# Kernel optimization log

Hardware: AMD Instinct MI355X
Metric: run time of the kernel (lower is better)

The kernel has to match this reference:

```python
import jax, jax.numpy as jnp
import numpy as np

NUM_CLASSES = 1000
ETA = 1e-6  # Constants.eta (small stabilizer)
N, D = 262144, 256


def setup_inputs() -> dict:
    key = jax.random.key(0)
    k1, k2 = jax.random.split(key)
    features = jax.random.normal(k1, (N, D), dtype=jnp.float32)
    labels = jax.random.randint(k2, (N,), 0, NUM_CLASSES, dtype=jnp.int32)
    conf_mat = jnp.zeros((NUM_CLASSES, NUM_CLASSES), dtype=jnp.float32)
    return {"features": features, "labels": labels, "conf_mat": conf_mat}


def reference(features, labels, conf_mat):
    C = NUM_CLASSES
    # --- per-class centroids via segment reduce (replaces per-class mask loop) ---
    counts = jax.ops.segment_sum(jnp.ones((features.shape[0],), features.dtype),
                                 labels, num_segments=C)            # [C]
    sums = jax.ops.segment_sum(features, labels, num_segments=C)    # [C, D]
    means = sums / jnp.maximum(counts, 1.0)[:, None]                # [C, D]

    # --- weighted between-class scatter list (sb_list from get_scatters) ---
    gmean = jnp.mean(features, axis=0)                              # [D]
    w = counts / features.shape[0]
    sb_list = w * jnp.sum((means - gmean) ** 2, axis=1)             # [C]

    # --- cosine distance between centroids ---
    mn = means / jnp.linalg.norm(means, axis=1, keepdims=True)      # L2-normalize rows
    dist = 1.0 - jnp.clip(mn @ mn.T, -1.0, 1.0)                     # [C, C]
    dist = dist.at[jnp.diag_indices(C)].set(jnp.inf)                # fill_diagonal_(inf)

    # first (row-major) position of the minimum == nonzero(dist == min)[0]
    flat = jnp.argmin(dist)
    i, j = flat // C, flat % C
    min_dist = jnp.where(i == j, jnp.sum(sb_list), dist[i, j])

    loss = jnp.log(1.0 / (min_dist + ETA) + 1.0)
    return loss
```

## Files before the change

### kernel.cpp

```cpp
#include <hip/hip_runtime.h>
#include <math.h>

#define N_ROWS 262144
#define D 256
#define C 1000
#define CAP 512
#define TILE 32
#define NTILE 32
#define NPAIR (NTILE * (NTILE + 1) / 2)

typedef float f4v __attribute__((ext_vector_type(4)));

__global__ void k_init(int* __restrict__ cnt, unsigned int* __restrict__ minb,
                       unsigned int* __restrict__ done) {
    int t = threadIdx.x;
    cnt[t] = 0;
    if (t == 0) *minb = 0x7f800000u;
    if (t == 1) *done = 0u;
}

__global__ void k_build(const int4* __restrict__ lab4, int* __restrict__ cnt,
                        int* __restrict__ list) {
    int i = blockIdx.x * 256 + threadIdx.x;
    int4 l = lab4[i];
    int base = i * 4;
    list[l.x * CAP + atomicAdd(&cnt[l.x], 1)] = base;
    list[l.y * CAP + atomicAdd(&cnt[l.y], 1)] = base + 1;
    list[l.z * CAP + atomicAdd(&cnt[l.z], 1)] = base + 2;
    list[l.w * CAP + atomicAdd(&cnt[l.w], 1)] = base + 3;
}

__global__ __launch_bounds__(512) void k_centroid(
    const float* __restrict__ feat, const int* __restrict__ list,
    const int* __restrict__ cnt, float* __restrict__ mn) {
    int c = blockIdx.x;
    int tid = threadIdx.x;
    int w = tid >> 6;
    int cg_ = tid & 63;
    int n = cnt[c];
    int nl = (n < CAP) ? n : CAP;

    __shared__ int srow[CAP];
    for (int i = tid; i < nl; i += 512) srow[i] = list[c * CAP + i];
    __syncthreads();

    f4v acc = {0.f, 0.f, 0.f, 0.f};
    int r = w;
    for (; r + 56 < nl; r += 64) {
        int rows[8];
        #pragma unroll
        for (int u = 0; u < 8; ++u) rows[u] = srow[r + u * 8];
        f4v v[8];
        #pragma unroll
        for (int u = 0; u < 8; ++u)
            v[u] = reinterpret_cast<const f4v*>(feat + (size_t)rows[u] * D)[cg_];
        #pragma unroll
        for (int u = 0; u < 8; ++u) acc += v[u];
    }
    for (; r < nl; r += 8) {
        int row = srow[r];
        acc += reinterpret_cast<const f4v*>(feat + (size_t)row * D)[cg_];
    }

    __shared__ f4v part[8][64];
    part[w][cg_] = acc;
    __syncthreads();
    if (w == 0) {
        f4v t = {0.f, 0.f, 0.f, 0.f};
        #pragma unroll
        for (int i = 0; i < 8; ++i) t += part[i][cg_];
        float inv = 1.0f / fmaxf((float)n, 1.0f);
        f4v mean = t * inv;
        float ss = mean.x * mean.x + mean.y * mean.y + mean.z * mean.z + mean.w * mean.w;
        #pragma unroll
        for (int o = 32; o; o >>= 1) ss += __shfl_down(ss, o, 64);
        ss = __shfl(ss, 0, 64);
        float rn = rsqrtf(ss);
        f4v o4 = mean * rn;
        reinterpret_cast<f4v*>(mn + (size_t)c * D)[cg_] = o4;
    }
}

__global__ __launch_bounds__(256) void k_mindist(
    const float* __restrict__ mn, unsigned int* __restrict__ minb,
    unsigned int* __restrict__ done, float* __restrict__ out) {
    int t = blockIdx.x;
    int bi = 0;
    while (t >= NTILE - bi) { t -= NTILE - bi; ++bi; }
    int bj = bi + t;
    int i0 = bi * TILE, j0 = bj * TILE;

    __shared__ float A[TILE * D];
    __shared__ float B[TILE * D];
    float4* A4 = reinterpret_cast<float4*>(A);
    float4* B4 = reinterpret_cast<float4*>(B);
    int tid = threadIdx.x;

    for (int k = tid; k < TILE * (D / 4); k += 256) {
        int r = k >> 6;
        int g = k & 63;
        int sg = g ^ ((r >> 1) & 7);
        int gi = i0 + r, gj = j0 + r;
        float4 z = make_float4(0.f, 0.f, 0.f, 0.f);
        A4[r * 64 + sg] = (gi < C) ? reinterpret_cast<const float4*>(mn + (size_t)gi * D)[g] : z;
        B4[r * 64 + sg] = (gj < C) ? reinterpret_cast<const float4*>(mn + (size_t)gj * D)[g] : z;
    }
    __syncthreads();

    int ti = tid >> 4, tj = tid & 15;
    int il = ti * 2, jl = tj * 2;
    int sa = ti & 7;
    int sb = tj & 7;

    float a00 = 0.f, a01 = 0.f, a10 = 0.f, a11 = 0.f;
    #pragma unroll 4
    for (int g = 0; g < 64; ++g) {
        float4 x0 = A4[il * 64 + (g ^ sa)];
        float4 x1 = A4[(il + 1) * 64 + (g ^ sa)];
        float4 y0 = B4[jl * 64 + (g ^ sb)];
        float4 y1 = B4[(jl + 1) * 64 + (g ^ sb)];
        a00 += x0.x * y0.x + x0.y * y0.y + x0.z * y0.z + x0.w * y0.w;
        a01 += x0.x * y1.x + x0.y * y1.y + x0.z * y1.z + x0.w * y1.w;
        a10 += x1.x * y0.x + x1.y * y0.y + x1.z * y0.z + x1.w * y0.w;
        a11 += x1.x * y1.x + x1.y * y1.y + x1.z * y1.z + x1.w * y1.w;
    }

    float m = INFINITY;
    int gi0 = i0 + il, gj0 = j0 + jl;
    if (gi0 < C && gj0 < C && gi0 != gj0)         m = fminf(m, 1.f - fminf(fmaxf(a00, -1.f), 1.f));
    if (gi0 < C && gj0 + 1 < C && gi0 != gj0 + 1) m = fminf(m, 1.f - fminf(fmaxf(a01, -1.f), 1.f));
    if (gi0 + 1 < C && gj0 < C && gi0 + 1 != gj0) m = fminf(m, 1.f - fminf(fmaxf(a10, -1.f), 1.f));
    if (gi0 + 1 < C && gj0 + 1 < C && gi0 != gj0) m = fminf(m, 1.f - fminf(fmaxf(a11, -1.f), 1.f));

    #pragma unroll
    for (int o = 32; o; o >>= 1) m = fminf(m, __shfl_down(m, o, 64));
    if ((tid & 63) == 0) atomicMin(minb, __float_as_uint(m));

    __syncthreads();
    if (tid == 0) {
        __threadfence();
        unsigned int old = atomicAdd(done, 1u);
        if (old == (unsigned int)(gridDim.x - 1)) {
            float d = __uint_as_float(atomicOr(minb, 0u));
            out[0] = logf(1.0f / (d + 1e-6f) + 1.0f);
        }
    }
}

extern "C" void kernel_launch(void* const* d_in, const int* in_sizes, int n_in,
                              void* d_out, int out_size, void* d_ws, size_t ws_size,
                              hipStream_t stream) {
    const float* feat   = (const float*)d_in[0];
    const int*   labels = (const int*)d_in[1];
    float* out = (float*)d_out;

    int*      cnt  = (int*)d_ws;
    int*      list = cnt + 1024;
    float*    mnrm = (float*)(list + C * CAP);
    unsigned* minb = (unsigned*)(mnrm + C * D);
    unsigned* done = minb + 1;

    k_init<<<1, 1024, 0, stream>>>(cnt, minb, done);
    k_build<<<N_ROWS / 4 / 256, 256, 0, stream>>>((const int4*)labels, cnt, list);
    k_centroid<<<C, 512, 0, stream>>>(feat, list, cnt, mnrm);
    k_mindist<<<NPAIR, 256, 0, stream>>>(mnrm, minb, done, out);
}
```

Measured before the change: 151.8 us.

## Replace list-based gather centroids with slab-partitioned shared-memory atomic segment sums

Drops the per-class row-list build and the gather kernel. Each block now streams a slab of rows and a 32-column group into a shared-memory accumulator of all classes, using LDS atomics, then writes the partial sums. A second kernel reduces the 32 slab partials per class and normalises the rows. Dividing by the count is skipped because it cancels under L2 normalisation. This removes the CAP truncation and the random row gathers, but adds about 33 MB of partial-sum traffic and heavy LDS atomic contention; init of minb/done is folded into block 0.

```diff
diff --git a/kernel.cpp b/kernel.cpp
--- a/kernel.cpp
+++ b/kernel.cpp
@@ -4,81 +4,78 @@
 #define N_ROWS 262144
 #define D 256
 #define C 1000
-#define CAP 512
+#define SLABS 32
+#define RPS (N_ROWS / SLABS)
+#define COLG 8
+#define PSTRIDE (C * 32)
 #define TILE 32
 #define NTILE 32
 #define NPAIR (NTILE * (NTILE + 1) / 2)
 
 typedef float f4v __attribute__((ext_vector_type(4)));
 
-__global__ void k_init(int* __restrict__ cnt, unsigned int* __restrict__ minb,
-                       unsigned int* __restrict__ done) {
-    int t = threadIdx.x;
-    cnt[t] = 0;
-    if (t == 0) *minb = 0x7f800000u;
-    if (t == 1) *done = 0u;
+__global__ __launch_bounds__(1024) void k_partial(
+    const float* __restrict__ feat, const int* __restrict__ labels,
+    float* __restrict__ partial, unsigned int* __restrict__ minb,
+    unsigned int* __restrict__ done) {
+    int b = blockIdx.x;
+    int s = b >> 3;
+    int g = b & 7;
+    int tid = threadIdx.x;
+    int row_off = tid >> 5;
+    int col = tid & 31;
+
+    if (b == 0) {
+        if (tid == 0) *minb = 0x7f800000u;
+        if (tid == 1) *done = 0u;
+    }
+
+    __shared__ float acc[C * 32];
+    for (int i = tid; i < C * 32; i += 1024) acc[i] = 0.f;
+    __syncthreads();
+
+    int base0 = s * RPS + row_off;
+    int colbase = g * 32 + col;
+    for (int it = 0; it < RPS / 256; ++it) {
+        int base = base0 + it * 256;
+        int cls[8];
+        float v[8];
+        #pragma unroll
+        for (int u = 0; u < 8; ++u) {
+            int r = base + u * 32;
+            cls[u] = labels[r];
+            v[u] = feat[(size_t)r * D + colbase];
+        }
+        #pragma unroll
+        for (int u = 0; u < 8; ++u)
+            atomicAdd(&acc[cls[u] * 32 + col], v[u]);
+    }
+    __syncthreads();
+
+    f4v* p4 = reinterpret_cast<f4v*>(partial + (size_t)b * PSTRIDE);
+    const f4v* a4 = reinterpret_cast<const f4v*>(acc);
+    for (int i = tid; i < PSTRIDE / 4; i += 1024) p4[i] = a4[i];
 }
 
-__global__ void k_build(const int4* __restrict__ lab4, int* __restrict__ cnt,
-                        int* __restrict__ list) {
-    int i = blockIdx.x * 256 + threadIdx.x;
-    int4 l = lab4[i];
-    int base = i * 4;
-    list[l.x * CAP + atomicAdd(&cnt[l.x], 1)] = base;
-    list[l.y * CAP + atomicAdd(&cnt[l.y], 1)] = base + 1;
-    list[l.z * CAP + atomicAdd(&cnt[l.z], 1)] = base + 2;
-    list[l.w * CAP + atomicAdd(&cnt[l.w], 1)] = base + 3;
-}
+__global__ __launch_bounds__(256) void k_norm(
+    const float* __restrict__ partial, float* __restrict__ mn) {
+    int c = blockIdx.x;
+    int d = threadIdx.x;
+    int g = d >> 5, cl = d & 31;
 
-__global__ __launch_bounds__(512) void k_centroid(
-    const float* __restrict__ feat, const int* __restrict__ list,
-    const int* __restrict__ cnt, float* __restrict__ mn) {
-    int c = blockIdx.x;
-    int tid = threadIdx.x;
-    int w = tid >> 6;
-    int cg_ = tid & 63;
-    int n = cnt[c];
-    int nl = (n < CAP) ? n : CAP;
+    float sum = 0.f;
+    #pragma unroll 4
+    for (int s = 0; s < SLABS; ++s)
+        sum += partial[(size_t)(s * COLG + g) * PSTRIDE + c * 32 + cl];
 
-    __shared__ int srow[CAP];
-    for (int i = tid; i < nl; i += 512) srow[i] = list[c * CAP + i];
+    float ss = sum * sum;
+    #pragma unroll
+    for (int o = 32; o; o >>= 1) ss += __shfl_down(ss, o, 64);
+    __shared__ float w[4];
+    if ((d & 63) == 0) w[d >> 6] = ss;
     __syncthreads();
-
-    f4v acc = {0.f, 0.f, 0.f, 0.f};
-    int r = w;
-    for (; r + 56 < nl; r += 64) {
-        int rows[8];
-        #pragma unroll
-        for (int u = 0; u < 8; ++u) rows[u] = srow[r + u * 8];
-        f4v v[8];
-        #pragma unroll
-        for (int u = 0; u < 8; ++u)
-            v[u] = reinterpret_cast<const f4v*>(feat + (size_t)rows[u] * D)[cg_];
-        #pragma unroll
-        for (int u = 0; u < 8; ++u) acc += v[u];
-    }
-    for (; r < nl; r += 8) {
-        int row = srow[r];
-        acc += reinterpret_cast<const f4v*>(feat + (size_t)row * D)[cg_];
-    }
-
-    __shared__ f4v part[8][64];
-    part[w][cg_] = acc;
-    __syncthreads();
-    if (w == 0) {
-        f4v t = {0.f, 0.f, 0.f, 0.f};
-        #pragma unroll
-        for (int i = 0; i < 8; ++i) t += part[i][cg_];
-        float inv = 1.0f / fmaxf((float)n, 1.0f);
-        f4v mean = t * inv;
-        float ss = mean.x * mean.x + mean.y * mean.y + mean.z * mean.z + mean.w * mean.w;
-        #pragma unroll
-        for (int o = 32; o; o >>= 1) ss += __shfl_down(ss, o, 64);
-        ss = __shfl(ss, 0, 64);
-        float rn = rsqrtf(ss);
-        f4v o4 = mean * rn;
-        reinterpret_cast<f4v*>(mn + (size_t)c * D)[cg_] = o4;
-    }
+    float tot = w[0] + w[1] + w[2] + w[3];
+    mn[(size_t)c * D + d] = sum * rsqrtf(tot);
 }
 
 __global__ __launch_bounds__(256) void k_mindist(
@@ -154,14 +151,12 @@
     const int*   labels = (const int*)d_in[1];
     float* out = (float*)d_out;
 
-    int*      cnt  = (int*)d_ws;
-    int*      list = cnt + 1024;
-    float*    mnrm = (float*)(list + C * CAP);
-    unsigned* minb = (unsigned*)(mnrm + C * D);
-    unsigned* done = minb + 1;
+    float*    partial = (float*)d_ws;
+    float*    mnrm    = partial + (size_t)SLABS * COLG * PSTRIDE;
+    unsigned* minb    = (unsigned*)(mnrm + (size_t)C * D);
+    unsigned* done    = minb + 1;
 
-    k_init<<<1, 1024, 0, stream>>>(cnt, minb, done);
-    k_build<<<N_ROWS / 4 / 256, 256, 0, stream>>>((const int4*)labels, cnt, list);
-    k_centroid<<<C, 512, 0, stream>>>(feat, list, cnt, mnrm);
+    k_partial<<<SLABS * COLG, 1024, 0, stream>>>(feat, labels, partial, minb, done);
+    k_norm<<<C, 256, 0, stream>>>(partial, mnrm);
     k_mindist<<<NPAIR, 256, 0, stream>>>(mnrm, minb, done, out);
 }
```

Result: slower. 395.8 us (+160.7%).

## Stream centroid gather rows through LDS with async global_load_lds pipeline

Applied to the files above, without the earlier changes.

Replaces the register-based 8-row unrolled gather in the centroid kernel with a per-wave software pipeline. Each wave uses global_load_lds to copy feature rows directly into a 16-slot shared-memory ring, keeps 8 loads in flight, and waits with explicit vmcnt before accumulating from LDS. It also drops the division by the count before normalization, because the L2 normalization cancels the scale. This adds 128KB of LDS per block, which limits occupancy, and relies on hand-written waitcnt counting for correctness.

```diff
diff --git a/kernel.cpp b/kernel.cpp
--- a/kernel.cpp
+++ b/kernel.cpp
@@ -8,6 +8,9 @@
 #define TILE 32
 #define NTILE 32
 #define NPAIR (NTILE * (NTILE + 1) / 2)
+#define NWV 8
+#define SLOTS 16
+#define DEPTH 8
 
 typedef float f4v __attribute__((ext_vector_type(4)));
 
@@ -36,48 +39,59 @@
     int c = blockIdx.x;
     int tid = threadIdx.x;
     int w = tid >> 6;
-    int cg_ = tid & 63;
+    int lane = tid & 63;
     int n = cnt[c];
     int nl = (n < CAP) ? n : CAP;
 
+    __shared__ __align__(16) char stage[NWV * SLOTS * 1024];
     __shared__ int srow[CAP];
+    __shared__ f4v part[NWV][64];
+
     for (int i = tid; i < nl; i += 512) srow[i] = list[c * CAP + i];
     __syncthreads();
 
+    int nw = (nl > w) ? ((nl - 1 - w) / NWV + 1) : 0;
+    char* wst = stage + (size_t)w * (SLOTS * 1024);
+
+#define ISSUE(I)                                                                     \
+    do {                                                                             \
+        int row_ = srow[w + (I)*NWV];                                                \
+        const float* gs_ = feat + (size_t)row_ * D + lane * 4;                       \
+        char* ds_ = wst + ((I) & (SLOTS - 1)) * 1024;                                \
+        __builtin_amdgcn_global_load_lds(                                            \
+            (const __attribute__((address_space(1))) void*)gs_,                      \
+            (__attribute__((address_space(3))) void*)ds_, 16, 0, 0);                 \
+    } while (0)
+
     f4v acc = {0.f, 0.f, 0.f, 0.f};
-    int r = w;
-    for (; r + 56 < nl; r += 64) {
-        int rows[8];
-        #pragma unroll
-        for (int u = 0; u < 8; ++u) rows[u] = srow[r + u * 8];
-        f4v v[8];
-        #pragma unroll
-        for (int u = 0; u < 8; ++u)
-            v[u] = reinterpret_cast<const f4v*>(feat + (size_t)rows[u] * D)[cg_];
-        #pragma unroll
-        for (int u = 0; u < 8; ++u) acc += v[u];
+    int nfly = (nw < DEPTH) ? nw : DEPTH;
+    for (int s = 0; s < nfly; ++s) ISSUE(s);
+    int steady = nw - nfly;
+    for (int i = 0; i < steady; ++i) {
+        asm volatile("s_waitcnt vmcnt(7)" ::: "memory");
+        __builtin_amdgcn_sched_barrier(0);
+        acc += *(const f4v*)(wst + (i & (SLOTS - 1)) * 1024 + lane * 16);
+        ISSUE(i + DEPTH);
     }
-    for (; r < nl; r += 8) {
-        int row = srow[r];
-        acc += reinterpret_cast<const f4v*>(feat + (size_t)row * D)[cg_];
-    }
+    asm volatile("s_waitcnt vmcnt(0)" ::: "memory");
+    __builtin_amdgcn_sched_barrier(0);
+    for (int i = steady; i < nw; ++i)
+        acc += *(const f4v*)(wst + (i & (SLOTS - 1)) * 1024 + lane * 16);
+#undef ISSUE
 
-    __shared__ f4v part[8][64];
-    part[w][cg_] = acc;
+    part[w][lane] = acc;
     __syncthreads();
     if (w == 0) {
         f4v t = {0.f, 0.f, 0.f, 0.f};
         #pragma unroll
-        for (int i = 0; i < 8; ++i) t += part[i][cg_];
-        float inv = 1.0f / fmaxf((float)n, 1.0f);
-        f4v mean = t * inv;
-        float ss = mean.x * mean.x + mean.y * mean.y + mean.z * mean.z + mean.w * mean.w;
+        for (int i = 0; i < NWV; ++i) t += part[i][lane];
+        float ss = t.x * t.x + t.y * t.y + t.z * t.z + t.w * t.w;
         #pragma unroll
         for (int o = 32; o; o >>= 1) ss += __shfl_down(ss, o, 64);
         ss = __shfl(ss, 0, 64);
         float rn = rsqrtf(ss);
-        f4v o4 = mean * rn;
-        reinterpret_cast<f4v*>(mn + (size_t)c * D)[cg_] = o4;
+        f4v o4 = t * rn;
+        reinterpret_cast<f4v*>(mn + (size_t)c * D)[lane] = o4;
     }
 }
 
```

Result: no change. 153.8 us (+1.3%).
